# Optimization experiments

Hardware: AMD Instinct MI355X
Metric: run time of the kernel (lower is better)

Reference implementation:

```python
import jax, jax.numpy as jnp
import numpy as np

RANK = 8
ALPHA = 16.0
SCALING = ALPHA / RANK  # 2.0
B, S, DIN, DOUT = 4, 4096, 4096, 4096


def setup_inputs() -> dict:
    key = jax.random.key(0)
    k = jax.random.split(key, 6)
    return {
        "x": jax.random.normal(k[0], (B, S, DIN), dtype=jnp.float32),
        "codes": jax.random.normal(k[1], (B, S, RANK), dtype=jnp.float32),
        "W": jax.random.normal(k[2], (DOUT, DIN), dtype=jnp.float32) * 0.02,
        "b": jax.random.normal(k[3], (DOUT,), dtype=jnp.float32) * 0.02,
        "lora_U": jax.random.normal(k[4], (DOUT, RANK), dtype=jnp.float32) * 0.02,
        "lora_V": jax.random.normal(k[5], (DIN, RANK), dtype=jnp.float32) * 0.02,
    }


def reference(x, codes, W, b, lora_U, lora_V):
    # base linear: x @ W^T + b  -> [B, S, DOUT]
    base = jnp.einsum("bsi,oi->bso", x, W) + b
    # generated low-rank update: (x @ V) gated by per-token codes, then @ U^T
    xv = jnp.einsum("bsi,ir->bsr", x, lora_V)          # [B, S, rank]
    lora = jnp.einsum("bsr,or->bso", xv * codes, lora_U)  # [B, S, DOUT]
    return base + lora * SCALING
```

## Files before the change

### kernel.cpp

```cpp
#include <hip/hip_runtime.h>
#include <hip/hip_bf16.h>


typedef __bf16 bf16_t;
typedef __bf16 bf16x8 __attribute__((ext_vector_type(8)));
typedef float f32x4 __attribute__((ext_vector_type(4)));

#define M_TOT 16384
#define N_TOT 4096
#define K_TOT 4096
#define NT 64

#define GLOAD_LDS16(gp, lp)                                                    \
  __builtin_amdgcn_global_load_lds(                                            \
      (const __attribute__((address_space(1))) void*)(gp),                     \
      (__attribute__((address_space(3))) void*)(lp), 16, 0, 0)

__global__ void __launch_bounds__(256) conv_w_kernel(const float* __restrict__ W,
                                                     bf16_t* __restrict__ wbf) {
  size_t i = ((size_t)blockIdx.x * 256 + threadIdx.x) * 8;
  const float4* p = (const float4*)(W + i);
  float4 a = p[0], b = p[1];
  bf16x8 v;
  v[0] = (bf16_t)a.x; v[1] = (bf16_t)a.y; v[2] = (bf16_t)a.z; v[3] = (bf16_t)a.w;
  v[4] = (bf16_t)b.x; v[5] = (bf16_t)b.y; v[6] = (bf16_t)b.z; v[7] = (bf16_t)b.w;
  *(bf16x8*)(wbf + i) = v;
}

__global__ void __launch_bounds__(256) prep_x_kernel(
    const float* __restrict__ x, const float* __restrict__ codes,
    const float* __restrict__ V, bf16_t* __restrict__ xbf,
    float* __restrict__ g) {
  const int tid = threadIdx.x;
  const int lane = tid & 63;
  const int wv = tid >> 6;
  const int m0 = blockIdx.x * 4;
  const int c0 = tid * 16;

  float xv[4][8];
#pragma unroll
  for (int rr = 0; rr < 4; ++rr)
#pragma unroll
    for (int r = 0; r < 8; ++r) xv[rr][r] = 0.f;

#pragma unroll
  for (int h = 0; h < 2; ++h) {
    const int cb = c0 + h * 8;
    float xr[4][8];
#pragma unroll
    for (int rr = 0; rr < 4; ++rr) {
      const float4* xp = (const float4*)(x + (size_t)(m0 + rr) * K_TOT + cb);
      float4 a0 = xp[0], a1 = xp[1];
      xr[rr][0] = a0.x; xr[rr][1] = a0.y; xr[rr][2] = a0.z; xr[rr][3] = a0.w;
      xr[rr][4] = a1.x; xr[rr][5] = a1.y; xr[rr][6] = a1.z; xr[rr][7] = a1.w;
      bf16x8 bv;
#pragma unroll
      for (int t = 0; t < 8; ++t) bv[t] = (bf16_t)xr[rr][t];
      *(bf16x8*)(xbf + (size_t)(m0 + rr) * K_TOT + cb) = bv;
    }
#pragma unroll
    for (int t = 0; t < 8; ++t) {
      const float4* vp = (const float4*)(V + (size_t)(cb + t) * 8);
      float4 v0 = vp[0], v1 = vp[1];
#pragma unroll
      for (int rr = 0; rr < 4; ++rr) {
        float xi = xr[rr][t];
        xv[rr][0] += xi * v0.x; xv[rr][1] += xi * v0.y;
        xv[rr][2] += xi * v0.z; xv[rr][3] += xi * v0.w;
        xv[rr][4] += xi * v1.x; xv[rr][5] += xi * v1.y;
        xv[rr][6] += xi * v1.z; xv[rr][7] += xi * v1.w;
      }
    }
  }

  __shared__ float red[4][4][8];
#pragma unroll
  for (int rr = 0; rr < 4; ++rr)
#pragma unroll
    for (int r = 0; r < 8; ++r) {
      float v = xv[rr][r];
      for (int s = 32; s > 0; s >>= 1) v += __shfl_down(v, s);
      if (lane == 0) red[wv][rr][r] = v;
    }
  __syncthreads();
  if (tid < 32) {
    int rr = tid >> 3, r = tid & 7;
    float tot = red[0][rr][r] + red[1][rr][r] + red[2][rr][r] + red[3][rr][r];
    int m = m0 + rr;
    g[m * 8 + r] = tot * codes[(size_t)m * 8 + r] * 2.0f;
  }
}


#define BAR __builtin_amdgcn_s_barrier()
#define VMC4 asm volatile("s_waitcnt vmcnt(4)" ::: "memory")
#define VMC0 asm volatile("s_waitcnt vmcnt(0)" ::: "memory")

#define STAGE(DB, AB, HALF, KT, SRC)                                           \
  {                                                                            \
    _Pragma("unroll") for (int r_ = 0; r_ < 2; ++r_) {                         \
      int rowl_ = (HALF) * 128 + (r_ * 8 + w) * 8 + srow;                      \
      const bf16_t* gp_ = (SRC) + (size_t)rowl_ * K_TOT + (KT) * 64 + sgk;     \
      GLOAD_LDS16(gp_, &lds[(DB) * 2 + (AB)][rowl_ * 64 + sj * 8]);            \
    }                                                                          \
  }

#define READ_A(BUF, MI0)                                                       \
  _Pragma("unroll") for (int mi_ = 0; mi_ < 4; ++mi_) {                        \
    aF[mi_][0] = *(const bf16x8*)&lds[(BUF) * 2][arow0 + ((MI0) + mi_) * 1024 + aslot0]; \
    aF[mi_][1] = *(const bf16x8*)&lds[(BUF) * 2][arow0 + ((MI0) + mi_) * 1024 + aslot1]; \
  }

#define READ_B(BUF, NJ0, DST)                                                  \
  _Pragma("unroll") for (int nj_ = 0; nj_ < 2; ++nj_) {                        \
    DST[nj_][0] = *(const bf16x8*)&lds[(BUF) * 2 + 1][brow0 + ((NJ0) + nj_) * 1024 + aslot0]; \
    DST[nj_][1] = *(const bf16x8*)&lds[(BUF) * 2 + 1][brow0 + ((NJ0) + nj_) * 1024 + aslot1]; \
  }

#define MFMA_Q(MI0, NJ0, BSRC)                                                 \
  __builtin_amdgcn_s_setprio(1);                                               \
  _Pragma("unroll") for (int mi_ = 0; mi_ < 4; ++mi_)                          \
  _Pragma("unroll") for (int nj_ = 0; nj_ < 2; ++nj_) {                        \
    acc[(MI0) + mi_][(NJ0) + nj_] = __builtin_amdgcn_mfma_f32_16x16x32_bf16(   \
        aF[mi_][0], BSRC[nj_][0], acc[(MI0) + mi_][(NJ0) + nj_], 0, 0, 0);     \
    acc[(MI0) + mi_][(NJ0) + nj_] = __builtin_amdgcn_mfma_f32_16x16x32_bf16(   \
        aF[mi_][1], BSRC[nj_][1], acc[(MI0) + mi_][(NJ0) + nj_], 0, 0, 0);     \
  }                                                                            \
  __builtin_amdgcn_s_setprio(0);

#define KTILE(BUF, KT, S1, S2, VMCW)                                           \
  if (S1) STAGE(BUF ^ 1, 0, 1, (KT) + 1, aSrc);                                \
  VMCW;                                                                        \
  BAR;                                                                         \
  READ_A(BUF, 0);                                                              \
  READ_B(BUF, 0, b01);                                                         \
  MFMA_Q(0, 0, b01);                                                           \
  BAR;                                                                         \
  if (S1) STAGE(BUF ^ 1, 1, 0, (KT) + 1, bSrc);                                \
  BAR;                                                                         \
  READ_B(BUF, 2, b23);                                                         \
  MFMA_Q(0, 2, b23);                                                           \
  BAR;                                                                         \
  if (S1) STAGE(BUF ^ 1, 1, 1, (KT) + 1, bSrc);                                \
  BAR;                                                                         \
  READ_A(BUF, 4);                                                              \
  MFMA_Q(4, 2, b23);                                                           \
  BAR;                                                                         \
  if (S2) STAGE(BUF, 0, 0, (KT) + 2, aSrc);                                    \
  BAR;                                                                         \
  MFMA_Q(4, 0, b01);                                                           \
  BAR;

__global__ void __launch_bounds__(512) gemm_kernel(
    const bf16_t* __restrict__ A,
    const bf16_t* __restrict__ Bm,
    const float* __restrict__ bias, const float* __restrict__ U,
    const float* __restrict__ g, float* __restrict__ out) {
  const int tid = threadIdx.x;
  const int lane = tid & 63;
  const int w = tid >> 6;
  const int wr = w >> 2;
  const int wc = w & 3;
  const int llo = lane & 15, lhi = lane >> 4;

  int bid = blockIdx.x;
  int sw = (bid & 7) * 128 + (bid >> 3);
  const int bm = sw >> 4;
  const int bn = sw & 15;

  __shared__ __attribute__((aligned(128))) bf16_t lds[4][16384];

  const bf16_t* aSrc = A + (size_t)bm * 256 * K_TOT;
  const bf16_t* bSrc = Bm + (size_t)bn * 256 * K_TOT;

  const int srow = lane >> 3;
  const int sj = lane & 7;
  const int sgk = (sj ^ srow) * 8;

  const int xs = llo & 7;
  const int arow0 = (wr * 128 + llo) * 64;
  const int brow0 = (wc * 64 + llo) * 64;
  const int aslot0 = ((0 + lhi) ^ xs) * 8;
  const int aslot1 = ((4 + lhi) ^ xs) * 8;

  f32x4 acc[8][4] = {};
  bf16x8 aF[4][2], b01[2][2], b23[2][2];

  STAGE(0, 0, 0, 0, aSrc);
  STAGE(0, 0, 1, 0, aSrc);
  STAGE(0, 1, 0, 0, bSrc);
  STAGE(0, 1, 1, 0, bSrc);
  STAGE(1, 0, 0, 1, aSrc);

#pragma unroll 1
  for (int t = 0; t < NT - 2; t += 2) {
    KTILE(0, t, 1, 1, VMC4);
    KTILE(1, t + 1, 1, 1, VMC4);
  }
  KTILE(0, NT - 2, 1, 0, VMC4);
  KTILE(1, NT - 1, 0, 0, VMC0);

  const int n0 = bn * 256 + wc * 64;
  int nidx[4];
  float biasv[4];
  float Un[4][8];
#pragma unroll
  for (int nj = 0; nj < 4; ++nj) {
    int n = n0 + nj * 16 + llo;
    nidx[nj] = n;
    biasv[nj] = bias[n];
    const float4* up = (const float4*)(U + (size_t)n * 8);
    float4 u0 = up[0], u1 = up[1];
    Un[nj][0] = u0.x; Un[nj][1] = u0.y; Un[nj][2] = u0.z; Un[nj][3] = u0.w;
    Un[nj][4] = u1.x; Un[nj][5] = u1.y; Un[nj][6] = u1.z; Un[nj][7] = u1.w;
  }
#pragma unroll
  for (int mi = 0; mi < 8; ++mi) {
#pragma unroll
    for (int reg = 0; reg < 4; ++reg) {
      int m = bm * 256 + wr * 128 + mi * 16 + lhi * 4 + reg;
      const float4* gp = (const float4*)(g + m * 8);
      float4 g0 = gp[0], g1 = gp[1];
      float* orow = out + (size_t)m * N_TOT;
#pragma unroll
      for (int nj = 0; nj < 4; ++nj) {
        float lora = g0.x * Un[nj][0] + g0.y * Un[nj][1] + g0.z * Un[nj][2] +
                     g0.w * Un[nj][3] + g1.x * Un[nj][4] + g1.y * Un[nj][5] +
                     g1.z * Un[nj][6] + g1.w * Un[nj][7];
        orow[nidx[nj]] = acc[mi][nj][reg] + biasv[nj] + lora;
      }
    }
  }
}

__global__ void __launch_bounds__(256) naive_kernel(
    const float* __restrict__ x, const float* __restrict__ codes,
    const float* __restrict__ W, const float* __restrict__ bias,
    const float* __restrict__ U, const float* __restrict__ V,
    float* __restrict__ out) {
  int m = blockIdx.x >> 4;
  int n = ((blockIdx.x & 15) << 8) + threadIdx.x;
  const float* xr = x + (size_t)m * K_TOT;
  const float* wrow = W + (size_t)n * K_TOT;
  float acc = 0.f;
  float xv[8] = {0, 0, 0, 0, 0, 0, 0, 0};
  for (int k = 0; k < K_TOT; k += 4) {
    float4 xa = *(const float4*)(xr + k);
    float4 wa = *(const float4*)(wrow + k);
    acc += xa.x * wa.x + xa.y * wa.y + xa.z * wa.z + xa.w * wa.w;
    const float* xs = (const float*)&xa;
#pragma unroll
    for (int t = 0; t < 4; ++t) {
      const float* vrow = V + (size_t)(k + t) * 8;
      float xi = xs[t];
#pragma unroll
      for (int r = 0; r < 8; ++r) xv[r] += xi * vrow[r];
    }
  }
  float lora = 0.f;
#pragma unroll
  for (int r = 0; r < 8; ++r)
    lora += xv[r] * codes[(size_t)m * 8 + r] * U[(size_t)n * 8 + r];
  out[(size_t)m * N_TOT + n] = acc + bias[n] + 2.0f * lora;
}

extern "C" void kernel_launch(void* const* d_in, const int* in_sizes, int n_in,
                              void* d_out, int out_size, void* d_ws,
                              size_t ws_size, hipStream_t stream) {
  const float* x = (const float*)d_in[0];
  const float* codes = (const float*)d_in[1];
  const float* W = (const float*)d_in[2];
  const float* b = (const float*)d_in[3];
  const float* U = (const float*)d_in[4];
  const float* V = (const float*)d_in[5];
  float* out = (float*)d_out;

  const size_t xbf_bytes = (size_t)M_TOT * K_TOT * 2;
  const size_t wbf_bytes = (size_t)N_TOT * K_TOT * 2;
  const size_t g_bytes = (size_t)M_TOT * 8 * 4;

  if (ws_size >= xbf_bytes + wbf_bytes + g_bytes) {
    bf16_t* xbf = (bf16_t*)d_ws;
    bf16_t* wbf = (bf16_t*)((char*)d_ws + xbf_bytes);
    float* g = (float*)((char*)d_ws + xbf_bytes + wbf_bytes);
    hipLaunchKernelGGL(conv_w_kernel, dim3(8192), dim3(256), 0, stream, W, wbf);
    hipLaunchKernelGGL(prep_x_kernel, dim3(4096), dim3(256), 0, stream, x,
                       codes, V, xbf, g);
    hipLaunchKernelGGL(gemm_kernel, dim3(1024), dim3(512), 0, stream, xbf, wbf,
                       b, U, g, out);
  } else {
    hipLaunchKernelGGL(naive_kernel, dim3((M_TOT) * (N_TOT / 256)), dim3(256),
                       0, stream, x, codes, W, b, U, V, out);
  }
}
```

Before: 627.4 us.

## Restructure K-tile pipeline to batch next-tile staging and move vmcnt wait

New measurement: 660.6 us. +5.3%, slower.

```diff
diff --git a/kernel.cpp b/kernel.cpp
--- a/kernel.cpp
+++ b/kernel.cpp
@@ -91,10 +91,10 @@
   }
 }
 
-
 #define BAR __builtin_amdgcn_s_barrier()
-#define VMC4 asm volatile("s_waitcnt vmcnt(4)" ::: "memory")
+#define VMC2 asm volatile("s_waitcnt vmcnt(2)" ::: "memory")
 #define VMC0 asm volatile("s_waitcnt vmcnt(0)" ::: "memory")
+#define LGKM0 asm volatile("s_waitcnt lgkmcnt(0)" ::: "memory")
 
 #define STAGE(DB, AB, HALF, KT, SRC)                                           \
   {                                                                            \
@@ -128,25 +128,27 @@
   }                                                                            \
   __builtin_amdgcn_s_setprio(0);
 
-#define KTILE(BUF, KT, S1, S2, VMCW)                                           \
-  if (S1) STAGE(BUF ^ 1, 0, 1, (KT) + 1, aSrc);                                \
-  VMCW;                                                                        \
-  BAR;                                                                         \
+#define KTILE(BUF, KT, S1, S2, VM)                                             \
   READ_A(BUF, 0);                                                              \
   READ_B(BUF, 0, b01);                                                         \
+  if (S1) {                                                                    \
+    STAGE(BUF ^ 1, 0, 1, (KT) + 1, aSrc);                                      \
+    STAGE(BUF ^ 1, 1, 0, (KT) + 1, bSrc);                                      \
+    STAGE(BUF ^ 1, 1, 1, (KT) + 1, bSrc);                                      \
+  }                                                                            \
+  BAR; LGKM0;                                                                  \
   MFMA_Q(0, 0, b01);                                                           \
   BAR;                                                                         \
-  if (S1) STAGE(BUF ^ 1, 1, 0, (KT) + 1, bSrc);                                \
-  BAR;                                                                         \
   READ_B(BUF, 2, b23);                                                         \
+  BAR; LGKM0;                                                                  \
   MFMA_Q(0, 2, b23);                                                           \
   BAR;                                                                         \
-  if (S1) STAGE(BUF ^ 1, 1, 1, (KT) + 1, bSrc);                                \
-  BAR;                                                                         \
   READ_A(BUF, 4);                                                              \
+  BAR; LGKM0;                                                                  \
   MFMA_Q(4, 2, b23);                                                           \
   BAR;                                                                         \
   if (S2) STAGE(BUF, 0, 0, (KT) + 2, aSrc);                                    \
+  if ((VM) == 2) { VMC2; } else if ((VM) == 0) { VMC0; }                       \
   BAR;                                                                         \
   MFMA_Q(4, 0, b01);                                                           \
   BAR;
@@ -191,14 +193,16 @@
   STAGE(0, 1, 0, 0, bSrc);
   STAGE(0, 1, 1, 0, bSrc);
   STAGE(1, 0, 0, 1, aSrc);
+  VMC2;
+  BAR;
 
 #pragma unroll 1
   for (int t = 0; t < NT - 2; t += 2) {
-    KTILE(0, t, 1, 1, VMC4);
-    KTILE(1, t + 1, 1, 1, VMC4);
-  }
-  KTILE(0, NT - 2, 1, 0, VMC4);
-  KTILE(1, NT - 1, 0, 0, VMC0);
+    KTILE(0, t, 1, 1, 2);
+    KTILE(1, t + 1, 1, 1, 2);
+  }
+  KTILE(0, NT - 2, 1, 0, 0);
+  KTILE(1, NT - 1, 0, 0, -1);
 
   const int n0 = bn * 256 + wc * 64;
   int nidx[4];
```
